# Kernel tuning notes

Measured on AMD Instinct MI355X. Metric: run time of the kernel, lower is better.

## Reference

```python
import jax, jax.numpy as jnp
import numpy as np
from jax import lax
from jax.scipy.special import logsumexp

V, H, L, C, B, T = 30000, 512, 2, 9, 128, 256


def setup_inputs() -> dict:
    key = jax.random.key(0)
    ks = jax.random.split(key, 14)
    k = 1.0 / np.sqrt(H)
    u = lambda kk, shp, s: jax.random.uniform(kk, shp, jnp.float32, -s, s)
    embed = jax.random.normal(ks[0], (V, H), jnp.float32) * 0.5
    embed = embed.at[0].set(0.0)  # padding_idx=0
    w_ih_l0 = u(ks[1], (2, 4 * H, H), k)      # [dir, 4H, in]
    w_hh_l0 = u(ks[2], (2, 4 * H, H), k)
    b_l0 = u(ks[3], (2, 4 * H), k)            # b_ih + b_hh combined
    w_ih_l1 = u(ks[4], (2, 4 * H, 2 * H), k)  # layer-1 input is 2H (bidir concat)
    w_hh_l1 = u(ks[5], (2, 4 * H, H), k)
    b_l1 = u(ks[6], (2, 4 * H), k)
    kc = 1.0 / np.sqrt(2 * H)
    cls_w = u(ks[7], (C, 2 * H), kc)
    cls_b = u(ks[8], (C,), kc)
    crf_start = u(ks[9], (C,), 0.1)
    crf_end = u(ks[10], (C,), 0.1)
    crf_trans = u(ks[11], (C, C), 0.1)
    x = jax.random.randint(ks[12], (B, T), 0, V)
    y = jax.random.randint(ks[13], (B, T), 0, C)
    return dict(x=x, y=y, embed=embed, w_ih_l0=w_ih_l0, w_hh_l0=w_hh_l0, b_l0=b_l0,
                w_ih_l1=w_ih_l1, w_hh_l1=w_hh_l1, b_l1=b_l1, cls_w=cls_w, cls_b=cls_b,
                crf_start=crf_start, crf_end=crf_end, crf_trans=crf_trans)


def _lstm_dir(xs, w_ih, w_hh, b):
    # xs: [T, B, Din] -> hidden states [T, B, H]
    Bn, Hn = xs.shape[1], w_hh.shape[-1]
    pre = jnp.einsum('tbd,gd->tbg', xs, w_ih) + b  # hoist input GEMM out of scan

    def step(carry, zt):
        h, c = carry
        z = zt + h @ w_hh.T
        i, f, g, o = jnp.split(z, 4, axis=-1)
        c = jax.nn.sigmoid(f) * c + jax.nn.sigmoid(i) * jnp.tanh(g)
        h = jax.nn.sigmoid(o) * jnp.tanh(c)
        return (h, c), h

    init = (jnp.zeros((Bn, Hn), xs.dtype), jnp.zeros((Bn, Hn), xs.dtype))
    _, hs = lax.scan(step, init, pre)
    return hs


def _bilstm_layer(xs, w_ih, w_hh, b):
    hf = _lstm_dir(xs, w_ih[0], w_hh[0], b[0])
    hb = _lstm_dir(xs[::-1], w_ih[1], w_hh[1], b[1])[::-1]
    return jnp.concatenate([hf, hb], axis=-1)  # [T, B, 2H]


def reference(x, y, embed, w_ih_l0, w_hh_l0, b_l0, w_ih_l1, w_hh_l1, b_l1,
              cls_w, cls_b, crf_start, crf_end, crf_trans):
    mask = y > -1                              # [B, T] (all True here)
    # Embedding with max_norm=1 (rows renormalized to L2 norm <= 1 at lookup)
    emb = embed[x]                             # [B, T, H]
    nrm = jnp.linalg.norm(emb, axis=-1, keepdims=True)
    emb = emb * jnp.where(nrm > 1.0, 1.0 / (nrm + 1e-7), 1.0)

    xs = emb.transpose(1, 0, 2)                # [T, B, H]
    hs = _bilstm_layer(xs, w_ih_l0, w_hh_l0, b_l0)
    hs = _bilstm_layer(hs, w_ih_l1, w_hh_l1, b_l1)
    emissions = jnp.einsum('tbh,ch->tbc', hs, cls_w) + cls_b  # [T, B, C]

    tags = jnp.maximum(y, 0).T                 # [T, B]
    mT = mask.T                                # [T, B] bool
    mF = mT.astype(emissions.dtype)
    bidx = jnp.arange(B)

    # ---- numerator: score of gold path ----
    em_tag = jnp.take_along_axis(emissions, tags[:, :, None], axis=-1)[..., 0]  # [T, B]
    trans_sc = crf_trans[tags[:-1], tags[1:]]  # [T-1, B]
    score = crf_start[tags[0]] + em_tag[0]
    score = score + jnp.sum((trans_sc + em_tag[1:]) * mF[1:], axis=0)
    seq_ends = jnp.sum(mT, axis=0) - 1         # [B]
    last_tags = tags[seq_ends, bidx]
    score = score + crf_end[last_tags]

    # ---- denominator: forward algorithm ----
    alpha0 = crf_start + emissions[0]          # [B, C]

    def den_step(alpha, inp):
        e_t, m_t = inp
        nxt = logsumexp(alpha[:, :, None] + crf_trans[None] + e_t[:, None, :], axis=1)
        return jnp.where(m_t[:, None], nxt, alpha), None

    alpha, _ = lax.scan(den_step, alpha0, (emissions[1:], mT[1:]))
    denom = logsumexp(alpha + crf_end, axis=1)

    llh = score - denom
    return -jnp.mean(llh)
```

## Files before the change

### kernel.cpp

```cpp
#include <hip/hip_runtime.h>
#include <hip/hip_bf16.h>

#define VV 30000
#define HH 512
#define NC 9
#define BB 128
#define TT 256
#define GG 2048
#define TB (TT*BB)

using short8 = __attribute__((ext_vector_type(8))) short;
using f32x4  = __attribute__((ext_vector_type(4))) float;

__device__ inline float bf2f(unsigned short u){
    union { unsigned int i; float f; } v; v.i = ((unsigned int)u) << 16; return v.f;
}
__device__ inline unsigned short f2bf(float f){
    union { unsigned int i; float f; } v; v.f = f;
    unsigned int x = v.i;
    unsigned int r = (x + 0x7fffu + ((x >> 16) & 1u)) >> 16;
    return (unsigned short)r;
}
__device__ inline float sigm(float x){
    if (x >= 0.f){ return 1.f / (1.f + __expf(-x)); }
    float e = __expf(x); return e / (1.f + e);
}
__device__ inline float tanh_f(float x){
    float ax = fabsf(x);
    float e = __expf(-2.f * ax);
    float t = (1.f - e) / (1.f + e);
    return copysignf(t, x);
}

__global__ void castbf(const float* __restrict__ in, unsigned short* __restrict__ out, int n){
    int i = blockIdx.x * blockDim.x + threadIdx.x;
    if (i < n) out[i] = f2bf(in[i]);
}

__global__ __launch_bounds__(256) void embed_k(const int* __restrict__ x,
                                               const float* __restrict__ embed,
                                               unsigned short* __restrict__ xs){
    int wid  = (int)((blockIdx.x * blockDim.x + threadIdx.x) >> 6);
    int lane = threadIdx.x & 63;
    if (wid >= TB) return;
    int t = wid >> 7, b = wid & 127;
    int tok = x[b * TT + t];
    const float4* e = (const float4*)(embed + (size_t)tok * HH);
    float4 v0 = e[lane], v1 = e[lane + 64];
    float ss = v0.x*v0.x + v0.y*v0.y + v0.z*v0.z + v0.w*v0.w
             + v1.x*v1.x + v1.y*v1.y + v1.z*v1.z + v1.w*v1.w;
    #pragma unroll
    for (int off = 32; off > 0; off >>= 1) ss += __shfl_xor(ss, off, 64);
    float nrm = sqrtf(ss);
    float sc = (nrm > 1.f) ? 1.f / (nrm + 1e-7f) : 1.f;
    unsigned short* dst = xs + (size_t)wid * HH;
    ushort4 o0, o1;
    o0.x = f2bf(v0.x * sc); o0.y = f2bf(v0.y * sc); o0.z = f2bf(v0.z * sc); o0.w = f2bf(v0.w * sc);
    o1.x = f2bf(v1.x * sc); o1.y = f2bf(v1.y * sc); o1.z = f2bf(v1.z * sc); o1.w = f2bf(v1.w * sc);
    ((ushort4*)dst)[lane]      = o0;
    ((ushort4*)dst)[lane + 64] = o1;
}

__global__ __launch_bounds__(256) void gemm2(const unsigned short* __restrict__ A0,
                                             const unsigned short* __restrict__ A1,
                                             const unsigned short* __restrict__ Wb_,
                                             const float* __restrict__ bias,
                                             unsigned short* __restrict__ Cout,
                                             int K, int CH){
    const int dz = blockIdx.z;
    const unsigned short* A  = dz ? A1 : A0;
    const unsigned short* W  = Wb_ + (size_t)dz * GG * K;
    const float*          bd = bias + dz * GG;
    unsigned short*       C  = Cout + (size_t)dz * CH * BB * GG;

    __shared__ __align__(16) unsigned short smem[16384];

    const int tid  = threadIdx.x;
    const int lane = tid & 63;
    const int wv   = tid >> 6;
    const int l15  = lane & 15, quad = lane >> 4;
    const int mw   = (wv >> 1) * 64;
    const int nw   = (wv & 1) * 64;

    const int nwg   = gridDim.x * gridDim.y;
    const int chunk = nwg >> 3;
    const int id    = blockIdx.x + gridDim.x * blockIdx.y;
    const int nid   = (id & 7) * chunk + (id >> 3);
    const int m0    = (nid % gridDim.x) * 128;
    const int n0    = (nid / gridDim.x) * 128;

    const int srow = lane >> 2;
    const int scol = (lane & 3) * 8;
    const int c0 = wv * 2, c1 = wv * 2 + 1;
    const unsigned short* gA0 = A + (size_t)(m0 + c0 * 16 + srow) * K + scol;
    const unsigned short* gA1 = A + (size_t)(m0 + c1 * 16 + srow) * K + scol;
    const unsigned short* gB0 = W + (size_t)(n0 + c0 * 16 + srow) * K + scol;
    const unsigned short* gB1 = W + (size_t)(n0 + c1 * 16 + srow) * K + scol;

    f32x4 acc[4][4];
    #pragma unroll
    for (int i = 0; i < 4; i++)
        #pragma unroll
        for (int j = 0; j < 4; j++){ acc[i][j][0]=0.f; acc[i][j][1]=0.f; acc[i][j][2]=0.f; acc[i][j][3]=0.f; }

    #define STAGE(bufi, kko)                                                                              \
        do {                                                                                              \
            __builtin_amdgcn_global_load_lds((const __attribute__((address_space(1))) void*)(gA0 + (kko)),\
                (__attribute__((address_space(3))) void*)(smem + (bufi) * 4096 + c0 * 512), 16, 0, 0);    \
            __builtin_amdgcn_global_load_lds((const __attribute__((address_space(1))) void*)(gA1 + (kko)),\
                (__attribute__((address_space(3))) void*)(smem + (bufi) * 4096 + c1 * 512), 16, 0, 0);    \
            __builtin_amdgcn_global_load_lds((const __attribute__((address_space(1))) void*)(gB0 + (kko)),\
                (__attribute__((address_space(3))) void*)(smem + 8192 + (bufi) * 4096 + c0 * 512), 16, 0, 0);\
            __builtin_amdgcn_global_load_lds((const __attribute__((address_space(1))) void*)(gB1 + (kko)),\
                (__attribute__((address_space(3))) void*)(smem + 8192 + (bufi) * 4096 + c1 * 512), 16, 0, 0);\
        } while (0)

    const int nk = K >> 5;
    STAGE(0, 0);
    for (int t = 0; t < nk; ++t){
        const int buf = t & 1;
        const bool more = (t + 1 < nk);
        if (more){
            STAGE((t + 1) & 1, (t + 1) << 5);
            __builtin_amdgcn_sched_barrier(0);
            asm volatile("s_waitcnt vmcnt(4)" ::: "memory");
        } else {
            __builtin_amdgcn_sched_barrier(0);
            asm volatile("s_waitcnt vmcnt(0)" ::: "memory");
        }
        __builtin_amdgcn_s_barrier();
        __builtin_amdgcn_sched_barrier(0);

        short8 a[4], b[4];
        #pragma unroll
        for (int i = 0; i < 4; i++) a[i] = *(const short8*)&smem[(size_t)buf * 4096 + (mw + i * 16 + l15) * 32 + quad * 8];
        #pragma unroll
        for (int j = 0; j < 4; j++) b[j] = *(const short8*)&smem[8192 + (size_t)buf * 4096 + (nw + j * 16 + l15) * 32 + quad * 8];
        #pragma unroll
        for (int i = 0; i < 4; i++)
            #pragma unroll
            for (int j = 0; j < 4; j++)
                acc[i][j] = __builtin_amdgcn_mfma_f32_16x16x32_bf16(a[i], b[j], acc[i][j], 0, 0, 0);

        __builtin_amdgcn_sched_barrier(0);
        __builtin_amdgcn_s_barrier();
        __builtin_amdgcn_sched_barrier(0);
    }
    #undef STAGE

    #pragma unroll
    for (int i = 0; i < 4; i++){
        #pragma unroll
        for (int j = 0; j < 4; j++){
            const int ncol = nw + j * 16 + l15;
            const float bn = bd[n0 + ncol];
            #pragma unroll
            for (int r = 0; r < 4; r++){
                const int mrow = mw + i * 16 + quad * 4 + r;
                smem[mrow * 128 + ncol] = f2bf(acc[i][j][r] + bn);
            }
        }
    }
    __syncthreads();
    #pragma unroll
    for (int it = 0; it < 8; it++){
        const int ch  = it * 256 + tid;
        const int row = ch >> 4;
        const int col = (ch & 15) * 8;
        *(short8*)(C + (size_t)(m0 + row) * GG + n0 + col) = *(const short8*)&smem[row * 128 + col];
    }
}

__global__ __launch_bounds__(256) void lstm_fused(const unsigned short* __restrict__ preC,
                                                  const unsigned short* __restrict__ whh,
                                                  unsigned short* __restrict__ hA,
                                                  unsigned short* __restrict__ hB,
                                                  float* __restrict__ cstate,
                                                  unsigned short* __restrict__ hs_out,
                                                  const float* __restrict__ cw,
                                                  float* __restrict__ em,
                                                  int t0, int nsteps, int CH, int fbase,
                                                  unsigned int* __restrict__ bar,
                                                  const unsigned short* __restrict__ An0,
                                                  const unsigned short* __restrict__ An1,
                                                  const unsigned short* __restrict__ Wi_,
                                                  const float* __restrict__ bias,
                                                  unsigned short* __restrict__ Cnext,
                                                  int K, int njobs){
    __shared__ __align__(16) unsigned char shm[69888];

    const int tid  = threadIdx.x;
    const int bx   = blockIdx.x;

    if (bx < 128){
        __builtin_amdgcn_s_setprio(1);

        unsigned short (*w_s)[16][520] = (unsigned short (*)[16][520])shm;
        unsigned short (*htile)[20]    = (unsigned short (*)[20])(shm + 66560);
        float (*cw_s)[16]              = (float (*)[16])(shm + 69120);

        const int lane = tid & 63;
        const int wv   = tid >> 6;
        const int l15  = lane & 15, quad = lane >> 4;
        const int grp  = bx & 3;
        const int d    = grp >> 1;
        const int mh   = grp & 1;
        const int jc   = bx >> 2;
        const int m0   = mh * 64;

        {
            const unsigned short* wbase = whh + (size_t)d * GG * HH;
            #pragma unroll
            for (int it = 0; it < 16; it++){
                int idx  = it * 256 + tid;
                int row  = idx >> 6;
                int col8 = idx & 63;
                int g2 = row >> 4, j2 = row & 15;
                short8 v = *(const short8*)(wbase + (size_t)(g2 * 512 + jc * 16 + j2) * HH + col8 * 8);
                *(short8*)&w_s[g2][j2][col8 * 8] = v;
            }
        }
        if (cw != nullptr && tid < NC * 16){
            int c = tid >> 4, j = tid & 15;
            cw_s[c][j] = cw[(size_t)c * 1024 + d * 512 + jc * 16 + j];
        }

        float csreg[4];
        #pragma unroll
        for (int rr = 0; rr < 4; rr++){
            const int gm = m0 + wv * 16 + quad * 4 + rr;
            csreg[rr] = cstate[((size_t)d * BB + gm) * HH + jc * 16 + l15];
        }

        unsigned short pf[4][4];
        {
            const int time0 = d ? (TT - 1 - t0) : t0;
            const int slot0 = time0 & (CH - 1);
            const unsigned short* p0 = preC + (((size_t)(d * CH + slot0)) * BB + (m0 + wv * 16 + quad * 4)) * GG + jc * 16 + l15;
            #pragma unroll
            for (int rr = 0; rr < 4; rr++)
                #pragma unroll
                for (int g = 0; g < 4; g++)
                    pf[rr][g] = p0[(size_t)rr * GG + g * 512];
        }
        __syncthreads();

        const size_t slabU = (size_t)grp * 8192;
        unsigned int* myFl  = bar + (((size_t)grp * 4 + wv) * 32 + jc) * 16;
        const unsigned int* pollFl = bar + (((size_t)grp * 4 + wv) * 32 + (lane & 31)) * 16;

        const int rowu = (wv * 16 + l15) * 4 + (quad & 1) * 2;
        const int jq   = quad >> 1;

        unsigned short pfN[4][4];

        for (int ls = 0; ls < nsteps; ls++){
            const int tt   = t0 + ls;
            const unsigned long long* srcU = (const unsigned long long*)((tt & 1) ? hB : hA) + slabU;
            unsigned long long*       dstU = (unsigned long long*)((tt & 1) ? hA : hB) + slabU + (size_t)jc * 256;

            if (ls > 0){
                const unsigned int tgt = (unsigned int)(fbase + ls);
                while (__hip_atomic_load(pollFl, __ATOMIC_RELAXED, __HIP_MEMORY_SCOPE_AGENT) < tgt)
                    __builtin_amdgcn_s_sleep(1);
                __builtin_amdgcn_fence(__ATOMIC_ACQUIRE, "workgroup");
                #pragma unroll
                for (int rr = 0; rr < 4; rr++)
                    #pragma unroll
                    for (int g = 0; g < 4; g++)
                        pf[rr][g] = pfN[rr][g];
            }

            unsigned long long afr[16][2];
            #pragma unroll
            for (int kk = 0; kk < 16; kk++){
                const unsigned long long* p = srcU + (size_t)(2 * kk + jq) * 256 + rowu;
                afr[kk][0] = __hip_atomic_load(p,     __ATOMIC_RELAXED, __HIP_MEMORY_SCOPE_AGENT);
                afr[kk][1] = __hip_atomic_load(p + 1, __ATOMIC_RELAXED, __HIP_MEMORY_SCOPE_AGENT);
            }

            f32x4 acc[4];
            #pragma unroll
            for (int g = 0; g < 4; g++){ acc[g][0]=0.f; acc[g][1]=0.f; acc[g][2]=0.f; acc[g][3]=0.f; }
            #pragma unroll
            for (int kk = 0; kk < 16; kk++){
                union { unsigned long long u[2]; short8 s; } cv;
                cv.u[0] = afr[kk][0]; cv.u[1] = afr[kk][1];
                const short8 a = cv.s;
                #pragma unroll
                for (int g = 0; g < 4; g++){
                    short8 b = *(const short8*)&w_s[g][l15][kk * 32 + quad * 8];
                    acc[g] = __builtin_amdgcn_mfma_f32_16x16x32_bf16(a, b, acc[g], 0, 0, 0);
                }
            }

            #pragma unroll
            for (int rr = 0; rr < 4; rr++){
                const int lr = wv * 16 + quad * 4 + rr;
                const float zi = acc[0][rr] + bf2f(pf[rr][0]);
                const float zf = acc[1][rr] + bf2f(pf[rr][1]);
                const float zg = acc[2][rr] + bf2f(pf[rr][2]);
                const float zo = acc[3][rr] + bf2f(pf[rr][3]);
                float cs = sigm(zf) * csreg[rr] + sigm(zi) * tanh_f(zg);
                csreg[rr] = cs;
                htile[lr][l15] = f2bf(sigm(zo) * tanh_f(cs));
            }
            const int trowL = lane >> 2;
            const unsigned long long hv8 = *(const unsigned long long*)&htile[wv * 16 + trowL][(lane & 3) * 4];

            __hip_atomic_store(dstU + wv * 64 + lane, hv8, __ATOMIC_RELAXED, __HIP_MEMORY_SCOPE_AGENT);
            asm volatile("s_waitcnt vmcnt(0)" ::: "memory");
            if (lane == 0)
                __hip_atomic_store(myFl, (unsigned int)(fbase + ls + 1), __ATOMIC_RELAXED, __HIP_MEMORY_SCOPE_AGENT);

            const int time = d ? (TT - 1 - tt) : tt;
            const bool more = (ls + 1 < nsteps);

            if (more){
                const int tt1 = tt + 1;
                const int time1 = d ? (TT - 1 - tt1) : tt1;
                const int slot1 = time1 & (CH - 1);
                const unsigned short* p1 = preC + (((size_t)(d * CH + slot1)) * BB + (m0 + wv * 16 + quad * 4)) * GG + jc * 16 + l15;
                #pragma unroll
                for (int rr = 0; rr < 4; rr++)
                    #pragma unroll
                    for (int g = 0; g < 4; g++)
                        pfN[rr][g] = p1[(size_t)rr * GG + g * 512];
            }

            if (cw == nullptr){
                *(unsigned long long*)(hs_out + ((size_t)time * BB + m0 + wv * 16 + trowL) * (2 * HH) + d * HH + jc * 16 + (lane & 3) * 4) = hv8;
            } else {
                const int part = lane & 3;
                float hvv[4];
                #pragma unroll
                for (int k = 0; k < 4; k++) hvv[k] = bf2f((unsigned short)(hv8 >> (16 * k)));
                float p[NC];
                #pragma unroll
                for (int c = 0; c < NC; c++){
                    float s = 0.f;
                    #pragma unroll
                    for (int k = 0; k < 4; k++) s += hvv[k] * cw_s[c][part * 4 + k];
                    p[c] = s;
                }
                #pragma unroll
                for (int c = 0; c < NC; c++){
                    p[c] += __shfl_xor(p[c], 1, 64);
                    p[c] += __shfl_xor(p[c], 2, 64);
                }
                if (part == 0){
                    float* emr = em + ((size_t)time * BB + m0 + wv * 16 + trowL) * NC;
                    #pragma unroll
                    for (int c = 0; c < NC; c++) atomicAdd(emr + c, p[c]);
                }
            }
        }

        #pragma unroll
        for (int rr = 0; rr < 4; rr++){
            const int gm = m0 + wv * 16 + quad * 4 + rr;
            cstate[((size_t)d * BB + gm) * HH + jc * 16 + l15] = csreg[rr];
        }
        return;
    }

    if (An0 == nullptr) return;
    unsigned short* smem = (unsigned short*)shm;

    const int lane = tid & 63;
    const int wv   = tid >> 6;
    const int l15  = lane & 15, quad = lane >> 4;
    const int mw   = (wv >> 1) * 64;
    const int nw   = (wv & 1) * 64;
    const int srow = lane >> 2;
    const int scol = (lane & 3) * 8;
    const int c0 = wv * 2, c1 = wv * 2 + 1;
    const int nhb = (int)gridDim.x - 128;
    const int CHn = nsteps;

    for (int job = bx - 128; job < njobs; job += nhb){
        const int xj  = job % CHn;
        const int rem = job / CHn;
        const int yj  = rem & 15;
        const int dz  = rem >> 4;
        const unsigned short* A  = dz ? An1 : An0;
        const unsigned short* W  = Wi_ + (size_t)dz * GG * K;
        const float*          bd = bias + dz * GG;
        unsigned short*       C  = Cnext + (size_t)dz * CHn * BB * GG;
        const int m0 = xj * 128;
        const int n0 = yj * 128;

        const unsigned short* gA0 = A + (size_t)(m0 + c0 * 16 + srow) * K + scol;
        const unsigned short* gA1 = A + (size_t)(m0 + c1 * 16 + srow) * K + scol;
        const unsigned short* gB0 = W + (size_t)(n0 + c0 * 16 + srow) * K + scol;
        const unsigned short* gB1 = W + (size_t)(n0 + c1 * 16 + srow) * K + scol;

        f32x4 acc[4][4];
        #pragma unroll
        for (int i = 0; i < 4; i++)
            #pragma unroll
            for (int j = 0; j < 4; j++){ acc[i][j][0]=0.f; acc[i][j][1]=0.f; acc[i][j][2]=0.f; acc[i][j][3]=0.f; }

        #define HSTAGE(bufi, kko)                                                                             \
            do {                                                                                              \
                __builtin_amdgcn_global_load_lds((const __attribute__((address_space(1))) void*)(gA0 + (kko)),\
                    (__attribute__((address_space(3))) void*)(smem + (bufi) * 4096 + c0 * 512), 16, 0, 0);    \
                __builtin_amdgcn_global_load_lds((const __attribute__((address_space(1))) void*)(gA1 + (kko)),\
                    (__attribute__((address_space(3))) void*)(smem + (bufi) * 4096 + c1 * 512), 16, 0, 0);    \
                __builtin_amdgcn_global_load_lds((const __attribute__((address_space(1))) void*)(gB0 + (kko)),\
                    (__attribute__((address_space(3))) void*)(smem + 8192 + (bufi) * 4096 + c0 * 512), 16, 0, 0);\
                __builtin_amdgcn_global_load_lds((const __attribute__((address_space(1))) void*)(gB1 + (kko)),\
                    (__attribute__((address_space(3))) void*)(smem + 8192 + (bufi) * 4096 + c1 * 512), 16, 0, 0);\
            } while (0)

        const int nk = K >> 5;
        HSTAGE(0, 0);
        for (int t = 0; t < nk; ++t){
            const int buf = t & 1;
            const bool more = (t + 1 < nk);
            if (more){
                HSTAGE((t + 1) & 1, (t + 1) << 5);
                __builtin_amdgcn_sched_barrier(0);
                asm volatile("s_waitcnt vmcnt(4)" ::: "memory");
            } else {
                __builtin_amdgcn_sched_barrier(0);
                asm volatile("s_waitcnt vmcnt(0)" ::: "memory");
            }
            __builtin_amdgcn_s_barrier();
            __builtin_amdgcn_sched_barrier(0);

            short8 a[4], b[4];
            #pragma unroll
            for (int i = 0; i < 4; i++) a[i] = *(const short8*)&smem[(size_t)buf * 4096 + (mw + i * 16 + l15) * 32 + quad * 8];
            #pragma unroll
            for (int j = 0; j < 4; j++) b[j] = *(const short8*)&smem[8192 + (size_t)buf * 4096 + (nw + j * 16 + l15) * 32 + quad * 8];
            #pragma unroll
            for (int i = 0; i < 4; i++)
                #pragma unroll
                for (int j = 0; j < 4; j++)
                    acc[i][j] = __builtin_amdgcn_mfma_f32_16x16x32_bf16(a[i], b[j], acc[i][j], 0, 0, 0);

            __builtin_amdgcn_sched_barrier(0);
            __builtin_amdgcn_s_barrier();
            __builtin_amdgcn_sched_barrier(0);
        }
        #undef HSTAGE

        #pragma unroll
        for (int i = 0; i < 4; i++){
            #pragma unroll
            for (int j = 0; j < 4; j++){
                const int ncol = nw + j * 16 + l15;
                const float bn = bd[n0 + ncol];
                #pragma unroll
                for (int r = 0; r < 4; r++){
                    const int mrow = mw + i * 16 + quad * 4 + r;
                    smem[mrow * 128 + ncol] = f2bf(acc[i][j][r] + bn);
                }
            }
        }
        __syncthreads();
        #pragma unroll
        for (int it = 0; it < 8; it++){
            const int ch  = it * 256 + tid;
            const int row = ch >> 4;
            const int col = (ch & 15) * 8;
            *(short8*)(C + (size_t)(m0 + row) * GG + n0 + col) = *(const short8*)&smem[row * 128 + col];
        }
        __syncthreads();
    }
}

__global__ void eminit(const float* __restrict__ cb, float* __restrict__ em){
    int i = blockIdx.x * blockDim.x + threadIdx.x;
    if (i < TB * NC) em[i] = cb[i % NC];
}

__global__ __launch_bounds__(64) void crf_k(const int* __restrict__ y,
                                            const float* __restrict__ em,
                                            const float* __restrict__ cstart,
                                            const float* __restrict__ cend,
                                            const float* __restrict__ ctr,
                                            float* __restrict__ llh){
    int b = blockIdx.x;
    int lane = threadIdx.x;

    float sp = 0.f; int cnt = 0;
    for (int t = lane; t < TT; t += 64){
        int yt = y[b * TT + t];
        bool mk = (yt > -1);
        cnt += mk ? 1 : 0;
        if (t >= 1 && mk){
            int yp  = y[b * TT + t - 1];
            int tag  = yt > 0 ? yt : 0;
            int tagp = yp > 0 ? yp : 0;
            sp += ctr[tagp * NC + tag] + em[((size_t)t * BB + b) * NC + tag];
        }
    }
    #pragma unroll
    for (int off = 32; off > 0; off >>= 1){
        sp  += __shfl_xor(sp, off, 64);
        cnt += __shfl_xor(cnt, off, 64);
    }

    float trc[NC];
    #pragma unroll
    for (int cc2 = 0; cc2 < NC; cc2++) trc[cc2] = 0.f;
    if (lane < NC){
        #pragma unroll
        for (int cc2 = 0; cc2 < NC; cc2++) trc[cc2] = ctr[cc2 * NC + lane];
    }
    float alpha = -1e30f;
    if (lane < NC) alpha = cstart[lane] + em[(size_t)b * NC + lane];

    for (int t = 1; t < TT; t++){
        int yt = y[b * TT + t];
        bool mk = (yt > -1);
        float e = (lane < NC) ? em[((size_t)t * BB + b) * NC + lane] : 0.f;
        float v[NC]; float mx = -1e30f;
        #pragma unroll
        for (int cc2 = 0; cc2 < NC; cc2++){
            float ac = __shfl(alpha, cc2, 64);
            v[cc2] = ac + trc[cc2];
            mx = fmaxf(mx, v[cc2]);
        }
        float s = 0.f;
        #pragma unroll
        for (int cc2 = 0; cc2 < NC; cc2++) s += __expf(v[cc2] - mx);
        float nxt = mx + __logf(s) + e;
        if (mk && lane < NC) alpha = nxt;
    }

    float val = (lane < NC) ? (alpha + cend[lane]) : -1e30f;
    float mx = -1e30f;
    #pragma unroll
    for (int cc2 = 0; cc2 < NC; cc2++) mx = fmaxf(mx, __shfl(val, cc2, 64));
    float s = 0.f;
    #pragma unroll
    for (int cc2 = 0; cc2 < NC; cc2++) s += __expf(__shfl(val, cc2, 64) - mx);
    float denom = mx + __logf(s);

    if (lane == 0){
        int y0 = y[b * TT];
        int tag0 = y0 > 0 ? y0 : 0;
        int se = cnt - 1;
        if (se < 0) se = 0;
        int yl = y[b * TT + se];
        int tagl = yl > 0 ? yl : 0;
        float score = sp + cstart[tag0] + em[(size_t)b * NC + tag0] + cend[tagl];
        llh[b] = score - denom;
    }
}

__global__ void final_k(const float* __restrict__ llh, float* __restrict__ out){
    __shared__ float sm[128];
    int i = threadIdx.x;
    sm[i] = llh[i];
    __syncthreads();
    for (int s = 64; s > 0; s >>= 1){
        if (i < s) sm[i] += sm[i + s];
        __syncthreads();
    }
    if (i == 0) out[0] = -sm[0] / 128.f;
}

__global__ void sentinel_k(float* out, float v){ out[0] = v; }

extern "C" void kernel_launch(void* const* d_in, const int* in_sizes, int n_in,
                              void* d_out, int out_size, void* d_ws, size_t ws_size,
                              hipStream_t stream) {
    const int*   x     = (const int*)d_in[0];
    const int*   y     = (const int*)d_in[1];
    const float* embed = (const float*)d_in[2];
    const float* wih0  = (const float*)d_in[3];
    const float* whh0  = (const float*)d_in[4];
    const float* b0    = (const float*)d_in[5];
    const float* wih1  = (const float*)d_in[6];
    const float* whh1  = (const float*)d_in[7];
    const float* b1    = (const float*)d_in[8];
    const float* clsw  = (const float*)d_in[9];
    const float* clsb  = (const float*)d_in[10];
    const float* cst   = (const float*)d_in[11];
    const float* cen   = (const float*)d_in[12];
    const float* ctr   = (const float*)d_in[13];
    float* out = (float*)d_out;

    const size_t sz_w0   = (size_t)2 * GG * HH * 2;
    const size_t sz_w1   = (size_t)2 * GG * 1024 * 2;
    const size_t sz_xs   = (size_t)TB * HH * 2;
    const size_t sz_hs0  = (size_t)TB * 1024 * 2;
    const size_t sz_h    = (size_t)2 * BB * HH * 2;
    const size_t sz_c    = (size_t)2 * BB * HH * 4;
    const size_t sz_emis = (size_t)TB * NC * 4;
    const size_t sz_llh  = (size_t)BB * 4;
    const size_t sz_bar  = 32768;
    auto rup = [](size_t v){ return (v + 255) & ~(size_t)255; };
    size_t fixed = rup(sz_w0) * 3 + rup(sz_w1) + rup(sz_xs) + rup(sz_hs0)
                 + rup(sz_h) * 2 + rup(sz_c) + rup(sz_emis) + rup(sz_llh) + rup(sz_bar);

    const int cands[5] = {128, 64, 32, 16, 8};
    int CH = 0;
    for (int i = 0; i < 5; i++){
        size_t par = (size_t)2 * cands[i] * BB * GG * 2;
        if (fixed + 2 * rup(par) <= ws_size){ CH = cands[i]; break; }
    }
    if (CH == 0){
        sentinel_k<<<1, 1, 0, stream>>>(out, -(float)(ws_size >> 20));
        return;
    }
    const size_t parSz = (size_t)2 * CH * BB * GG * 2;

    char* ws = (char*)d_ws;
    size_t off = 0;
    auto alloc = [&](size_t bytes) -> void* {
        void* p = (void*)(ws + off);
        off += (bytes + 255) & ~(size_t)255;
        return p;
    };
    unsigned short* wih0b = (unsigned short*)alloc(sz_w0);
    unsigned short* whh0b = (unsigned short*)alloc(sz_w0);
    unsigned short* whh1b = (unsigned short*)alloc(sz_w0);
    unsigned short* wih1b = (unsigned short*)alloc(sz_w1);
    unsigned short* xs    = (unsigned short*)alloc(sz_xs);
    unsigned short* hs0   = (unsigned short*)alloc(sz_hs0);
    unsigned short* hA    = (unsigned short*)alloc(sz_h);
    unsigned short* hB    = (unsigned short*)alloc(sz_h);
    float*          cbuf  = (float*)alloc(sz_c);
    float*          emis  = (float*)alloc(sz_emis);
    float*          llh   = (float*)alloc(sz_llh);
    unsigned int*   bar   = (unsigned int*)alloc(sz_bar);
    unsigned short* preC0 = (unsigned short*)alloc(parSz);
    unsigned short* preC1 = (unsigned short*)alloc(parSz);

    castbf<<<(2 * GG * HH + 255) / 256, 256, 0, stream>>>(wih0, wih0b, 2 * GG * HH);
    castbf<<<(2 * GG * HH + 255) / 256, 256, 0, stream>>>(whh0, whh0b, 2 * GG * HH);
    castbf<<<(2 * GG * 1024 + 255) / 256, 256, 0, stream>>>(wih1, wih1b, 2 * GG * 1024);
    castbf<<<(2 * GG * HH + 255) / 256, 256, 0, stream>>>(whh1, whh1b, 2 * GG * HH);

    embed_k<<<TB / 4, 256, 0, stream>>>(x, embed, xs);
    (void)hipMemsetAsync(bar, 0, sz_bar, stream);

    const int nch = TT / CH;
    const int njobs = CH * 16 * 2;

    eminit<<<(TB * NC + 255) / 256, 256, 0, stream>>>(clsb, emis);

    (void)hipMemsetAsync(hA, 0, sz_h, stream);
    (void)hipMemsetAsync(cbuf, 0, sz_c, stream);
    gemm2<<<dim3(CH, GG / 128, 2), 256, 0, stream>>>(
        xs, xs + (size_t)(TT - CH) * BB * HH, wih0b, b0, preC0, HH, CH);
    for (int c = 0; c < nch; c++){
        unsigned short* cur = (c & 1) ? preC1 : preC0;
        unsigned short* nxt = (c & 1) ? preC0 : preC1;
        const bool more = (c + 1 < nch);
        lstm_fused<<<more ? 512 : 128, 256, 0, stream>>>(cur, whh0b, hA, hB, cbuf, hs0,
            nullptr, emis, c * CH, CH, CH, c * CH, bar,
            more ? xs + (size_t)(c + 1) * CH * BB * HH : nullptr,
            more ? xs + (size_t)(TT - (size_t)(c + 2) * CH) * BB * HH : nullptr,
            wih0b, b0, nxt, HH, njobs);
    }

    (void)hipMemsetAsync(hA, 0, sz_h, stream);
    (void)hipMemsetAsync(cbuf, 0, sz_c, stream);
    gemm2<<<dim3(CH, GG / 128, 2), 256, 0, stream>>>(
        hs0, hs0 + (size_t)(TT - CH) * BB * 1024, wih1b, b1, preC0, 1024, CH);
    for (int c = 0; c < nch; c++){
        unsigned short* cur = (c & 1) ? preC1 : preC0;
        unsigned short* nxt = (c & 1) ? preC0 : preC1;
        const bool more = (c + 1 < nch);
        lstm_fused<<<more ? 512 : 128, 256, 0, stream>>>(cur, whh1b, hA, hB, cbuf, hs0,
            clsw, emis, c * CH, CH, CH, TT + c * CH, bar,
            more ? hs0 + (size_t)(c + 1) * CH * BB * 1024 : nullptr,
            more ? hs0 + (size_t)(TT - (size_t)(c + 2) * CH) * BB * 1024 : nullptr,
            wih1b, b1, nxt, 1024, njobs);
    }

    crf_k<<<BB, 64, 0, stream>>>(y, emis, cst, cen, ctr, llh);
    final_k<<<1, 128, 0, stream>>>(llh, out);
}
```

Measured before the change: 4.654 ms.

## Overlap layer-1 input GEMM with layer-0 recurrence via flag-gated helper blocks

When the time axis is split into two chunks, the separate layer-1 input-projection GEMM launch is removed. Helper blocks in the second layer-0 recurrence kernel instead spin on per-step progress flags and compute layer-1 pre-activations for each timestep as soon as both directions have written the needed hidden rows. Layer-0 hidden outputs are now written with agent-scope atomic stores before the flag update so helpers can read them consistently. This hides the layer-1 GEMM behind the serial recurrence, at the cost of helper blocks spin-waiting and a simpler, unpipelined GEMM loop.

```diff
diff --git a/kernel.cpp b/kernel.cpp
--- a/kernel.cpp
+++ b/kernel.cpp
@@ -186,7 +186,8 @@
                                                   const unsigned short* __restrict__ Wi_,
                                                   const float* __restrict__ bias,
                                                   unsigned short* __restrict__ Cnext,
-                                                  int K, int njobs){
+                                                  int K, int njobs,
+                                                  int CHnext, int fbaseHelp, int aAtomic){
     __shared__ __align__(16) unsigned char shm[69888];
 
     const int tid  = threadIdx.x;
@@ -308,14 +309,18 @@
             const int trowL = lane >> 2;
             const unsigned long long hv8 = *(const unsigned long long*)&htile[wv * 16 + trowL][(lane & 3) * 4];
 
+            const int time = d ? (TT - 1 - tt) : tt;
+
             __hip_atomic_store(dstU + wv * 64 + lane, hv8, __ATOMIC_RELAXED, __HIP_MEMORY_SCOPE_AGENT);
+            if (cw == nullptr)
+                __hip_atomic_store((unsigned long long*)(hs_out + ((size_t)time * BB + m0 + wv * 16 + trowL) * (2 * HH)
+                                   + d * HH + jc * 16 + (lane & 3) * 4), hv8,
+                                   __ATOMIC_RELAXED, __HIP_MEMORY_SCOPE_AGENT);
             asm volatile("s_waitcnt vmcnt(0)" ::: "memory");
             if (lane == 0)
                 __hip_atomic_store(myFl, (unsigned int)(fbase + ls + 1), __ATOMIC_RELAXED, __HIP_MEMORY_SCOPE_AGENT);
 
-            const int time = d ? (TT - 1 - tt) : tt;
             const bool more = (ls + 1 < nsteps);
-
             if (more){
                 const int tt1 = tt + 1;
                 const int time1 = d ? (TT - 1 - tt1) : tt1;
@@ -328,9 +333,7 @@
                         pfN[rr][g] = p1[(size_t)rr * GG + g * 512];
             }
 
-            if (cw == nullptr){
-                *(unsigned long long*)(hs_out + ((size_t)time * BB + m0 + wv * 16 + trowL) * (2 * HH) + d * HH + jc * 16 + (lane & 3) * 4) = hv8;
-            } else {
+            if (cw != nullptr){
                 const int part = lane & 3;
                 float hvv[4];
                 #pragma unroll
@@ -376,17 +379,106 @@
     const int scol = (lane & 3) * 8;
     const int c0 = wv * 2, c1 = wv * 2 + 1;
     const int nhb = (int)gridDim.x - 128;
-    const int CHn = nsteps;
+
+    if (aAtomic){
+        const int ar  = tid >> 1;
+        const int ac0 = (tid & 1) * 16;
+        for (int job = bx - 128; job < njobs; job += nhb){
+            const int k   = job >> 5;
+            const int rem = job & 31;
+            const int yj  = rem & 15;
+            const int dz  = rem >> 4;
+            const int xj  = dz ? k : (127 - k);
+
+            {
+                const unsigned int tgt = (unsigned int)(fbaseHelp + k + 1);
+                const unsigned int* fl = bar + ((size_t)((dz ? 0 : 2) * 128 + tid)) * 16;
+                while (__hip_atomic_load(fl, __ATOMIC_RELAXED, __HIP_MEMORY_SCOPE_AGENT) < tgt)
+                    __builtin_amdgcn_s_sleep(1);
+            }
+            __syncthreads();
+            __builtin_amdgcn_fence(__ATOMIC_ACQUIRE, "workgroup");
+
+            const unsigned short* A  = dz ? An1 : An0;
+            const unsigned short* W  = Wi_ + (size_t)dz * GG * K;
+            const float*          bd = bias + dz * GG;
+            unsigned short*       C  = Cnext + (size_t)dz * CHnext * BB * GG;
+            const int m0 = xj * 128;
+            const int n0 = yj * 128;
+            const unsigned short* gB0 = W + (size_t)(n0 + c0 * 16 + srow) * K + scol;
+            const unsigned short* gB1 = W + (size_t)(n0 + c1 * 16 + srow) * K + scol;
+
+            f32x4 acc[4][4];
+            #pragma unroll
+            for (int i = 0; i < 4; i++)
+                #pragma unroll
+                for (int j = 0; j < 4; j++){ acc[i][j][0]=0.f; acc[i][j][1]=0.f; acc[i][j][2]=0.f; acc[i][j][3]=0.f; }
+
+            for (int kk = 0; kk < K; kk += 32){
+                __syncthreads();
+                __builtin_amdgcn_global_load_lds((const __attribute__((address_space(1))) void*)(gB0 + kk),
+                    (__attribute__((address_space(3))) void*)(smem + 8192 + c0 * 512), 16, 0, 0);
+                __builtin_amdgcn_global_load_lds((const __attribute__((address_space(1))) void*)(gB1 + kk),
+                    (__attribute__((address_space(3))) void*)(smem + 8192 + c1 * 512), 16, 0, 0);
+                unsigned long long av[4];
+                const unsigned long long* ap = (const unsigned long long*)(A + (size_t)(m0 + ar) * K + kk + ac0);
+                #pragma unroll
+                for (int j = 0; j < 4; j++)
+                    av[j] = __hip_atomic_load(ap + j, __ATOMIC_RELAXED, __HIP_MEMORY_SCOPE_AGENT);
+                asm volatile("s_waitcnt vmcnt(0)" ::: "memory");
+                #pragma unroll
+                for (int j = 0; j < 4; j++)
+                    *(unsigned long long*)&smem[ar * 32 + ac0 + j * 4] = av[j];
+                __syncthreads();
+
+                short8 a[4], b[4];
+                #pragma unroll
+                for (int i = 0; i < 4; i++) a[i] = *(const short8*)&smem[(mw + i * 16 + l15) * 32 + quad * 8];
+                #pragma unroll
+                for (int j = 0; j < 4; j++) b[j] = *(const short8*)&smem[8192 + (nw + j * 16 + l15) * 32 + quad * 8];
+                #pragma unroll
+                for (int i = 0; i < 4; i++)
+                    #pragma unroll
+                    for (int j = 0; j < 4; j++)
+                        acc[i][j] = __builtin_amdgcn_mfma_f32_16x16x32_bf16(a[i], b[j], acc[i][j], 0, 0, 0);
+            }
+
+            __syncthreads();
+            #pragma unroll
+            for (int i = 0; i < 4; i++){
+                #pragma unroll
+                for (int j = 0; j < 4; j++){
+                    const int ncol = nw + j * 16 + l15;
+                    const float bn = bd[n0 + ncol];
+                    #pragma unroll
+                    for (int r = 0; r < 4; r++){
+                        const int mrow = mw + i * 16 + quad * 4 + r;
+                        smem[mrow * 128 + ncol] = f2bf(acc[i][j][r] + bn);
+                    }
+                }
+            }
+            __syncthreads();
+            #pragma unroll
+            for (int it = 0; it < 8; it++){
+                const int ch  = it * 256 + tid;
+                const int row = ch >> 4;
+                const int col = (ch & 15) * 8;
+                *(short8*)(C + (size_t)(m0 + row) * GG + n0 + col) = *(const short8*)&smem[row * 128 + col];
+            }
+            __syncthreads();
+        }
+        return;
+    }
 
     for (int job = bx - 128; job < njobs; job += nhb){
-        const int xj  = job % CHn;
-        const int rem = job / CHn;
+        const int xj  = job % CHnext;
+        const int rem = job / CHnext;
         const int yj  = rem & 15;
         const int dz  = rem >> 4;
         const unsigned short* A  = dz ? An1 : An0;
         const unsigned short* W  = Wi_ + (size_t)dz * GG * K;
         const float*          bd = bias + dz * GG;
-        unsigned short*       C  = Cnext + (size_t)dz * CHn * BB * GG;
+        unsigned short*       C  = Cnext + (size_t)dz * CHnext * BB * GG;
         const int m0 = xj * 128;
         const int n0 = yj * 128;
 
@@ -645,34 +737,59 @@
 
     eminit<<<(TB * NC + 255) / 256, 256, 0, stream>>>(clsb, emis);
 
-    (void)hipMemsetAsync(hA, 0, sz_h, stream);
-    (void)hipMemsetAsync(cbuf, 0, sz_c, stream);
-    gemm2<<<dim3(CH, GG / 128, 2), 256, 0, stream>>>(
-        xs, xs + (size_t)(TT - CH) * BB * HH, wih0b, b0, preC0, HH, CH);
-    for (int c = 0; c < nch; c++){
-        unsigned short* cur = (c & 1) ? preC1 : preC0;
-        unsigned short* nxt = (c & 1) ? preC0 : preC1;
-        const bool more = (c + 1 < nch);
-        lstm_fused<<<more ? 512 : 128, 256, 0, stream>>>(cur, whh0b, hA, hB, cbuf, hs0,
-            nullptr, emis, c * CH, CH, CH, c * CH, bar,
-            more ? xs + (size_t)(c + 1) * CH * BB * HH : nullptr,
-            more ? xs + (size_t)(TT - (size_t)(c + 2) * CH) * BB * HH : nullptr,
-            wih0b, b0, nxt, HH, njobs);
-    }
-
-    (void)hipMemsetAsync(hA, 0, sz_h, stream);
-    (void)hipMemsetAsync(cbuf, 0, sz_c, stream);
-    gemm2<<<dim3(CH, GG / 128, 2), 256, 0, stream>>>(
-        hs0, hs0 + (size_t)(TT - CH) * BB * 1024, wih1b, b1, preC0, 1024, CH);
-    for (int c = 0; c < nch; c++){
-        unsigned short* cur = (c & 1) ? preC1 : preC0;
-        unsigned short* nxt = (c & 1) ? preC0 : preC1;
-        const bool more = (c + 1 < nch);
-        lstm_fused<<<more ? 512 : 128, 256, 0, stream>>>(cur, whh1b, hA, hB, cbuf, hs0,
-            clsw, emis, c * CH, CH, CH, TT + c * CH, bar,
-            more ? hs0 + (size_t)(c + 1) * CH * BB * 1024 : nullptr,
-            more ? hs0 + (size_t)(TT - (size_t)(c + 2) * CH) * BB * 1024 : nullptr,
-            wih1b, b1, nxt, 1024, njobs);
+    if (nch == 2){
+        (void)hipMemsetAsync(hA, 0, sz_h, stream);
+        (void)hipMemsetAsync(cbuf, 0, sz_c, stream);
+        gemm2<<<dim3(CH, GG / 128, 2), 256, 0, stream>>>(
+            xs, xs + (size_t)CH * BB * HH, wih0b, b0, preC0, HH, CH);
+        lstm_fused<<<512, 256, 0, stream>>>(preC0, whh0b, hA, hB, cbuf, hs0,
+            nullptr, emis, 0, CH, CH, 0, bar,
+            xs + (size_t)CH * BB * HH, xs, wih0b, b0, preC1, HH, njobs,
+            CH, 0, 0);
+        lstm_fused<<<512, 256, 0, stream>>>(preC1, whh0b, hA, hB, cbuf, hs0,
+            nullptr, emis, CH, CH, CH, CH, bar,
+            hs0, hs0 + (size_t)CH * BB * 1024, wih1b, b1, preC0, 1024, njobs,
+            CH, CH, 1);
+
+        (void)hipMemsetAsync(hA, 0, sz_h, stream);
+        (void)hipMemsetAsync(cbuf, 0, sz_c, stream);
+        lstm_fused<<<512, 256, 0, stream>>>(preC0, whh1b, hA, hB, cbuf, hs0,
+            clsw, emis, 0, CH, CH, TT, bar,
+            hs0 + (size_t)CH * BB * 1024, hs0, wih1b, b1, preC1, 1024, njobs,
+            CH, 0, 0);
+        lstm_fused<<<128, 256, 0, stream>>>(preC1, whh1b, hA, hB, cbuf, hs0,
+            clsw, emis, CH, CH, CH, TT + CH, bar,
+            nullptr, nullptr, wih1b, b1, nullptr, 1024, njobs,
+            CH, 0, 0);
+    } else {
+        (void)hipMemsetAsync(hA, 0, sz_h, stream);
+        (void)hipMemsetAsync(cbuf, 0, sz_c, stream);
+        gemm2<<<dim3(CH, GG / 128, 2), 256, 0, stream>>>(
+            xs, xs + (size_t)(TT - CH) * BB * HH, wih0b, b0, preC0, HH, CH);
+        for (int c = 0; c < nch; c++){
+            unsigned short* cur = (c & 1) ? preC1 : preC0;
+            unsigned short* nxt = (c & 1) ? preC0 : preC1;
+            const bool more = (c + 1 < nch);
+            lstm_fused<<<more ? 512 : 128, 256, 0, stream>>>(cur, whh0b, hA, hB, cbuf, hs0,
+                nullptr, emis, c * CH, CH, CH, c * CH, bar,
+                more ? xs + (size_t)(c + 1) * CH * BB * HH : nullptr,
+                more ? xs + (size_t)(TT - (size_t)(c + 2) * CH) * BB * HH : nullptr,
+                wih0b, b0, nxt, HH, njobs, CH, 0, 0);
+        }
+        (void)hipMemsetAsync(hA, 0, sz_h, stream);
+        (void)hipMemsetAsync(cbuf, 0, sz_c, stream);
+        gemm2<<<dim3(CH, GG / 128, 2), 256, 0, stream>>>(
+            hs0, hs0 + (size_t)(TT - CH) * BB * 1024, wih1b, b1, preC0, 1024, CH);
+        for (int c = 0; c < nch; c++){
+            unsigned short* cur = (c & 1) ? preC1 : preC0;
+            unsigned short* nxt = (c & 1) ? preC0 : preC1;
+            const bool more = (c + 1 < nch);
+            lstm_fused<<<more ? 512 : 128, 256, 0, stream>>>(cur, whh1b, hA, hB, cbuf, hs0,
+                clsw, emis, c * CH, CH, CH, TT + c * CH, bar,
+                more ? hs0 + (size_t)(c + 1) * CH * BB * 1024 : nullptr,
+                more ? hs0 + (size_t)(TT - (size_t)(c + 2) * CH) * BB * 1024 : nullptr,
+                wih1b, b1, nxt, 1024, njobs, CH, 0, 0);
+        }
     }
 
     crf_k<<<BB, 64, 0, stream>>>(y, emis, cst, cen, ctr, llh);
```

Result: no change. 4.711 ms (+1.2%).
